# Optimization experiments

Measured on AMD Instinct MI355X. Metric: run time of the kernel, lower is better.

The kernel has to match this reference:

```python
import jax, jax.numpy as jnp
import numpy as np

ATTENTION_DIM = 256
TEMPERATURE = 1.0
NEG_INF = -2.0**32 + 1.0  # matches tf code's padding value


def setup_inputs() -> dict:
    key = jax.random.key(0)
    k1, k2, k3, k4, k5, k6, k7 = jax.random.split(key, 7)
    B, Q, M, QD, MD, AD, VD = 8, 2048, 2048, 512, 512, 256, 256
    inputs = jax.random.normal(k1, (B, Q, QD), dtype=jnp.float32)
    memory = jax.random.normal(k2, (B, M, MD), dtype=jnp.float32)
    memory_lengths = jnp.maximum(jax.random.randint(k3, (B,), 0, M + 1), 1).astype(jnp.int32)
    query_lengths = jnp.maximum(jax.random.randint(k4, (B,), 0, Q + 1), 1).astype(jnp.int32)
    s = 0.02
    Wq = jax.random.normal(k5, (QD, AD), dtype=jnp.float32) * s
    Wk = jax.random.normal(k6, (MD, AD), dtype=jnp.float32) * s
    Wv = jax.random.normal(k7, (MD, VD), dtype=jnp.float32) * s
    return {"inputs": inputs, "memory": memory, "memory_lengths": memory_lengths,
            "query_lengths": query_lengths, "Wq": Wq, "Wk": Wk, "Wv": Wv}


def reference(inputs, memory, memory_lengths, query_lengths, Wq, Wk, Wv):
    # Dense projections (no bias). NOTE: original code (faithfully reproduced)
    # computes values with the KEY layer; Wv is unused.
    queries = jnp.einsum('bqd,da->bqa', inputs, Wq)   # [B,Q,AD]
    keys = jnp.einsum('bmd,da->bma', memory, Wk)      # [B,M,AD]
    values = jnp.einsum('bmd,da->bma', memory, Wk)    # [B,M,AD] (bug in source)

    logits = jnp.einsum('bqa,bma->bqm', queries, keys)
    logits = logits / jnp.sqrt(jnp.float32(ATTENTION_DIM)) / TEMPERATURE

    B, Q, _ = inputs.shape
    M = memory.shape[1]
    mem_mask = jnp.arange(M)[None, :] < memory_lengths[:, None]   # [B,M]
    qry_mask = jnp.arange(Q)[None, :] < query_lengths[:, None]    # [B,Q]
    length_mask = qry_mask[:, :, None] & mem_mask[:, None, :]     # [B,Q,M]

    logits = jnp.where(length_mask, logits, jnp.float32(NEG_INF))
    alignments = jax.nn.softmax(logits, axis=2)                   # [B,Q,M]
    contexts = jnp.einsum('bqm,bma->bqa', alignments, values)     # [B,Q,AD]
    return contexts, alignments
```

## Files before the change

kernel.cpp:

```cpp
#include <hip/hip_runtime.h>
#include <hip/hip_bf16.h>

typedef __attribute__((ext_vector_type(8))) short s8v;
typedef __attribute__((ext_vector_type(4))) float f4v;
typedef __attribute__((ext_vector_type(4))) unsigned short us4;
typedef unsigned short u16;

__device__ __forceinline__ u16 f2bf(float f) {
  union { float f; unsigned int u; } x;
  x.f = f;
  unsigned int lsb = (x.u >> 16) & 1u;
  return (u16)((x.u + 0x7fffu + lsb) >> 16);
}

__device__ __forceinline__ uint4 pack8(float4 a, float4 b) {
  union { u16 u[8]; uint4 v; } t;
  t.u[0] = f2bf(a.x); t.u[1] = f2bf(a.y); t.u[2] = f2bf(a.z); t.u[3] = f2bf(a.w);
  t.u[4] = f2bf(b.x); t.u[5] = f2bf(b.y); t.u[6] = f2bf(b.z); t.u[7] = f2bf(b.w);
  return t.v;
}

__global__ __launch_bounds__(256) void proj_kernel(
    const float* __restrict__ inputs, const float* __restrict__ memory,
    const float* __restrict__ Wq, const float* __restrict__ Wk,
    u16* __restrict__ qb, u16* __restrict__ krow, u16* __restrict__ kcol)
{
  __shared__ u16 Wt[64 * 264];
  __shared__ u16 At[64 * 40];

  const int tid = threadIdx.x;
  const int w = tid >> 6;
  const int l = tid & 63;
  const int lr = l & 15;
  const int lh = l >> 4;
  const int rbase = blockIdx.x * 64;
  const int n0 = blockIdx.y * 64;
  const int src = blockIdx.z;
  const float* __restrict__ A  = src ? memory : inputs;
  const float* __restrict__ Wg = src ? Wk : Wq;

  f4v acc[4];
#pragma unroll
  for (int i = 0; i < 4; ++i) acc[i] = f4v{0.f, 0.f, 0.f, 0.f};

  for (int kh = 0; kh < 2; ++kh) {
    {
      const int kl = tid >> 3;
      const int nl = (tid & 7) * 8;
#pragma unroll
      for (int i = 0; i < 8; ++i) {
        const int k = kl + i * 32;
        const float* s = Wg + (size_t)(kh * 256 + k) * 256 + n0 + nl;
        float4 x0 = *(const float4*)s;
        float4 x1 = *(const float4*)(s + 4);
        Wt[(nl + 0) * 264 + k] = f2bf(x0.x);
        Wt[(nl + 1) * 264 + k] = f2bf(x0.y);
        Wt[(nl + 2) * 264 + k] = f2bf(x0.z);
        Wt[(nl + 3) * 264 + k] = f2bf(x0.w);
        Wt[(nl + 4) * 264 + k] = f2bf(x1.x);
        Wt[(nl + 5) * 264 + k] = f2bf(x1.y);
        Wt[(nl + 6) * 264 + k] = f2bf(x1.z);
        Wt[(nl + 7) * 264 + k] = f2bf(x1.w);
      }
    }
    __syncthreads();
    for (int ks = 0; ks < 8; ++ks) {
      {
        const int row = tid >> 2;
        const int kk = (tid & 3) * 8;
        const float* s = A + (size_t)(rbase + row) * 512 + kh * 256 + ks * 32 + kk;
        float4 x0 = *(const float4*)s;
        float4 x1 = *(const float4*)(s + 4);
        *(uint4*)&At[row * 40 + kk] = pack8(x0, x1);
      }
      __syncthreads();
      const s8v af = *(const s8v*)&At[(w * 16 + lr) * 40 + lh * 8];
#pragma unroll
      for (int nt = 0; nt < 4; ++nt) {
        const s8v bf = *(const s8v*)&Wt[(nt * 16 + lr) * 264 + ks * 32 + lh * 8];
        acc[nt] = __builtin_amdgcn_mfma_f32_16x16x32_bf16(af, bf, acc[nt], 0, 0, 0);
      }
      __syncthreads();
    }
  }

  u16* __restrict__ dst = src ? krow : qb;
#pragma unroll
  for (int nt = 0; nt < 4; ++nt) {
    const int col = n0 + nt * 16 + lr;
    const int R0 = rbase + w * 16 + lh * 4;
    u16 u0 = f2bf(acc[nt][0]);
    u16 u1 = f2bf(acc[nt][1]);
    u16 u2 = f2bf(acc[nt][2]);
    u16 u3 = f2bf(acc[nt][3]);
    dst[(size_t)(R0 + 0) * 256 + col] = u0;
    dst[(size_t)(R0 + 1) * 256 + col] = u1;
    dst[(size_t)(R0 + 2) * 256 + col] = u2;
    dst[(size_t)(R0 + 3) * 256 + col] = u3;
    if (src) {
      const int bb = R0 >> 11;
      const int mm = R0 & 2047;
      us4 pk;
      pk[0] = u0; pk[1] = u1; pk[2] = u2; pk[3] = u3;
      *(us4*)&kcol[((size_t)bb * 256 + col) * 2048 + mm] = pk;
    }
  }
}

__global__ __launch_bounds__(256) void attn_kernel(
    const u16* __restrict__ qb, const u16* __restrict__ krow,
    const u16* __restrict__ kcol, const int* __restrict__ mlens,
    const int* __restrict__ qlens, float* __restrict__ out_ctx,
    float* __restrict__ out_align, float* __restrict__ invsum)
{
  __shared__ u16 kr[32 * 264];
  __shared__ u16 kc[256 * 40];
  __shared__ u16 pl[4 * 16 * 40];

  const int tid = threadIdx.x;
  const int w = tid >> 6;
  const int l = tid & 63;
  const int lr = l & 15;
  const int lh = l >> 4;
  const int b = blockIdx.y;
  const int q0 = blockIdx.x * 64;
  const int mlen = mlens[b];
  const int qlen = qlens[b];
  const int qrow0 = q0 + w * 16 + lh * 4;

  s8v qf[8];
  {
    const u16* qp = qb + ((size_t)b * 2048 + q0 + w * 16 + lr) * 256 + lh * 8;
#pragma unroll
    for (int s = 0; s < 8; ++s) qf[s] = *(const s8v*)(qp + s * 32);
  }

  f4v oacc[16];
#pragma unroll
  for (int i = 0; i < 16; ++i) oacc[i] = f4v{0.f, 0.f, 0.f, 0.f};
  float psum[4] = {0.f, 0.f, 0.f, 0.f};

  const float C2 = 0.09016844005556021f;

  for (int m0 = 0; m0 < 2048; m0 += 32) {
#pragma unroll
    for (int i = 0; i < 4; ++i) {
      const int idx = i * 256 + tid;
      const int m = idx >> 5, G = idx & 31;
      uint4 v = *(const uint4*)(krow + (((size_t)b * 2048 + m0 + m) << 8) + G * 8);
      *(uint4*)&kr[m * 264 + G * 8] = v;
      const int a2 = idx >> 2, gm = idx & 3;
      uint4 v2 = *(const uint4*)(kcol + (((size_t)b * 256 + a2) << 11) + m0 + gm * 8);
      *(uint4*)&kc[a2 * 40 + gm * 8] = v2;
    }
    __syncthreads();

    f4v sacc[2];
    sacc[0] = f4v{0.f, 0.f, 0.f, 0.f};
    sacc[1] = f4v{0.f, 0.f, 0.f, 0.f};
#pragma unroll
    for (int s = 0; s < 8; ++s) {
#pragma unroll
      for (int f = 0; f < 2; ++f) {
        const s8v bf = *(const s8v*)&kr[(f * 16 + lr) * 264 + s * 32 + lh * 8];
        sacc[f] = __builtin_amdgcn_mfma_f32_16x16x32_bf16(qf[s], bf, sacc[f], 0, 0, 0);
      }
    }

#pragma unroll
    for (int f = 0; f < 2; ++f) {
      const int m = m0 + f * 16 + lr;
      const bool vm = m < mlen;
#pragma unroll
      for (int r = 0; r < 4; ++r) {
        const int q = qrow0 + r;
        float p = exp2f(sacc[f][r] * C2);
        if (!vm) p = 0.f;
        if (q >= qlen) p = 1.f;
        psum[r] += p;
        out_align[((size_t)b * 2048 + q) * 2048 + m] = p;
        pl[w * 640 + (lh * 4 + r) * 40 + f * 16 + lr] = f2bf(p);
      }
    }

    const s8v pa = *(const s8v*)&pl[w * 640 + lr * 40 + lh * 8];
#pragma unroll
    for (int at = 0; at < 16; ++at) {
      const s8v vf = *(const s8v*)&kc[(at * 16 + lr) * 40 + lh * 8];
      oacc[at] = __builtin_amdgcn_mfma_f32_16x16x32_bf16(pa, vf, oacc[at], 0, 0, 0);
    }
    __syncthreads();
  }

#pragma unroll
  for (int r = 0; r < 4; ++r) {
    float v = psum[r];
    v += __shfl_xor(v, 1);
    v += __shfl_xor(v, 2);
    v += __shfl_xor(v, 4);
    v += __shfl_xor(v, 8);
    psum[r] = 1.0f / v;
  }

#pragma unroll
  for (int at = 0; at < 16; ++at) {
    const int a = at * 16 + lr;
#pragma unroll
    for (int r = 0; r < 4; ++r) {
      out_ctx[((size_t)b * 2048 + qrow0 + r) * 256 + a] = oacc[at][r] * psum[r];
    }
  }
  if (lr == 0) {
#pragma unroll
    for (int r = 0; r < 4; ++r) invsum[(size_t)b * 2048 + qrow0 + r] = psum[r];
  }
}

__global__ __launch_bounds__(256) void norm_kernel(
    float* __restrict__ align, const float* __restrict__ invsum)
{
  const int row = blockIdx.x;
  const float inv = invsum[row];
  float4* p = (float4*)(align + (size_t)row * 2048);
  const int t = threadIdx.x;
#pragma unroll
  for (int i = 0; i < 2; ++i) {
    float4 v = p[i * 256 + t];
    v.x *= inv; v.y *= inv; v.z *= inv; v.w *= inv;
    p[i * 256 + t] = v;
  }
}

extern "C" void kernel_launch(void* const* d_in, const int* in_sizes, int n_in,
                              void* d_out, int out_size, void* d_ws, size_t ws_size,
                              hipStream_t stream) {
  const float* inputs = (const float*)d_in[0];
  const float* memory = (const float*)d_in[1];
  const int* mlens    = (const int*)d_in[2];
  const int* qlens    = (const int*)d_in[3];
  const float* Wq     = (const float*)d_in[4];
  const float* Wk     = (const float*)d_in[5];
  (void)in_sizes; (void)n_in; (void)out_size; (void)ws_size;

  u16* wsu = (u16*)d_ws;
  u16* qb   = wsu;
  u16* krow = wsu + 4194304;
  u16* kcol = wsu + 8388608;
  float* invsum = (float*)(wsu + 12582912);

  float* out_ctx = (float*)d_out;
  float* out_align = out_ctx + 4194304;

  proj_kernel<<<dim3(256, 4, 2), dim3(256), 0, stream>>>(
      inputs, memory, Wq, Wk, qb, krow, kcol);
  attn_kernel<<<dim3(32, 8), dim3(256), 0, stream>>>(
      qb, krow, kcol, mlens, qlens, out_ctx, out_align, invsum);
  norm_kernel<<<dim3(16384), dim3(256), 0, stream>>>(out_align, invsum);
}
```

Baseline: 201.8 us.

## Split attention into sum pass and split-M write pass, dropping normalize pass

```diff
diff --git a/kernel.cpp b/kernel.cpp
--- a/kernel.cpp
+++ b/kernel.cpp
@@ -107,15 +107,12 @@
   }
 }
 
-__global__ __launch_bounds__(256) void attn_kernel(
+__global__ __launch_bounds__(256) void attn_sum_kernel(
     const u16* __restrict__ qb, const u16* __restrict__ krow,
-    const u16* __restrict__ kcol, const int* __restrict__ mlens,
-    const int* __restrict__ qlens, float* __restrict__ out_ctx,
-    float* __restrict__ out_align, float* __restrict__ invsum)
+    const int* __restrict__ mlens, const int* __restrict__ qlens,
+    float* __restrict__ psum_p)
 {
   __shared__ u16 kr[32 * 264];
-  __shared__ u16 kc[256 * 40];
-  __shared__ u16 pl[4 * 16 * 40];
 
   const int tid = threadIdx.x;
   const int w = tid >> 6;
@@ -124,6 +121,8 @@
   const int lh = l >> 4;
   const int b = blockIdx.y;
   const int q0 = blockIdx.x * 64;
+  const int ms = blockIdx.z;
+  const int m_base = ms * 512;
   const int mlen = mlens[b];
   const int qlen = qlens[b];
   const int qrow0 = q0 + w * 16 + lh * 4;
@@ -135,14 +134,109 @@
     for (int s = 0; s < 8; ++s) qf[s] = *(const s8v*)(qp + s * 32);
   }
 
+  float psum[4] = {0.f, 0.f, 0.f, 0.f};
+  const float C2 = 0.09016844005556021f;
+
+  for (int mo = 0; mo < 512; mo += 32) {
+    const int m0 = m_base + mo;
+#pragma unroll
+    for (int i = 0; i < 4; ++i) {
+      const int idx = i * 256 + tid;
+      const int m = idx >> 5, G = idx & 31;
+      uint4 v = *(const uint4*)(krow + (((size_t)b * 2048 + m0 + m) << 8) + G * 8);
+      *(uint4*)&kr[m * 264 + G * 8] = v;
+    }
+    __syncthreads();
+
+    f4v sacc[2];
+    sacc[0] = f4v{0.f, 0.f, 0.f, 0.f};
+    sacc[1] = f4v{0.f, 0.f, 0.f, 0.f};
+#pragma unroll
+    for (int s = 0; s < 8; ++s) {
+#pragma unroll
+      for (int f = 0; f < 2; ++f) {
+        const s8v bf = *(const s8v*)&kr[(f * 16 + lr) * 264 + s * 32 + lh * 8];
+        sacc[f] = __builtin_amdgcn_mfma_f32_16x16x32_bf16(qf[s], bf, sacc[f], 0, 0, 0);
+      }
+    }
+#pragma unroll
+    for (int f = 0; f < 2; ++f) {
+      const int m = m0 + f * 16 + lr;
+      const bool vm = m < mlen;
+#pragma unroll
+      for (int r = 0; r < 4; ++r) {
+        float p = exp2f(sacc[f][r] * C2);
+        if (!vm) p = 0.f;
+        if (qrow0 + r >= qlen) p = 1.f;
+        psum[r] += p;
+      }
+    }
+    __syncthreads();
+  }
+
+#pragma unroll
+  for (int r = 0; r < 4; ++r) {
+    float v = psum[r];
+    v += __shfl_xor(v, 1);
+    v += __shfl_xor(v, 2);
+    v += __shfl_xor(v, 4);
+    v += __shfl_xor(v, 8);
+    psum[r] = v;
+  }
+  if (lr == 0) {
+#pragma unroll
+    for (int r = 0; r < 4; ++r)
+      psum_p[ms * 16384 + b * 2048 + qrow0 + r] = psum[r];
+  }
+}
+
+__global__ __launch_bounds__(256) void attn_wr_kernel(
+    const u16* __restrict__ qb, const u16* __restrict__ krow,
+    const u16* __restrict__ kcol, const int* __restrict__ mlens,
+    const int* __restrict__ qlens, const float* __restrict__ psum_p,
+    float* __restrict__ out_align, float* __restrict__ octx0,
+    float* __restrict__ octx1)
+{
+  __shared__ u16 kr[32 * 264];
+  __shared__ u16 kc[256 * 40];
+  __shared__ u16 pl[4 * 16 * 40];
+
+  const int tid = threadIdx.x;
+  const int w = tid >> 6;
+  const int l = tid & 63;
+  const int lr = l & 15;
+  const int lh = l >> 4;
+  const int b = blockIdx.y;
+  const int q0 = blockIdx.x * 64;
+  const int mh = blockIdx.z;
+  const int m_base = mh * 1024;
+  const int mlen = mlens[b];
+  const int qlen = qlens[b];
+  const int qrow0 = q0 + w * 16 + lh * 4;
+
+  s8v qf[8];
+  {
+    const u16* qp = qb + ((size_t)b * 2048 + q0 + w * 16 + lr) * 256 + lh * 8;
+#pragma unroll
+    for (int s = 0; s < 8; ++s) qf[s] = *(const s8v*)(qp + s * 32);
+  }
+
+  float inv[4];
+#pragma unroll
+  for (int r = 0; r < 4; ++r) {
+    const int q = b * 2048 + qrow0 + r;
+    float s = psum_p[q] + psum_p[16384 + q] + psum_p[32768 + q] + psum_p[49152 + q];
+    inv[r] = 1.0f / s;
+  }
+
   f4v oacc[16];
 #pragma unroll
   for (int i = 0; i < 16; ++i) oacc[i] = f4v{0.f, 0.f, 0.f, 0.f};
-  float psum[4] = {0.f, 0.f, 0.f, 0.f};
 
   const float C2 = 0.09016844005556021f;
 
-  for (int m0 = 0; m0 < 2048; m0 += 32) {
+  for (int mo = 0; mo < 1024; mo += 32) {
+    const int m0 = m_base + mo;
 #pragma unroll
     for (int i = 0; i < 4; ++i) {
       const int idx = i * 256 + tid;
@@ -177,9 +271,9 @@
         float p = exp2f(sacc[f][r] * C2);
         if (!vm) p = 0.f;
         if (q >= qlen) p = 1.f;
-        psum[r] += p;
-        out_align[((size_t)b * 2048 + q) * 2048 + m] = p;
-        pl[w * 640 + (lh * 4 + r) * 40 + f * 16 + lr] = f2bf(p);
+        const float pn = p * inv[r];
+        __builtin_nontemporal_store(pn, &out_align[((size_t)b * 2048 + q) * 2048 + m]);
+        pl[w * 640 + (lh * 4 + r) * 40 + f * 16 + lr] = f2bf(pn);
       }
     }
 
@@ -192,43 +286,26 @@
     __syncthreads();
   }
 
-#pragma unroll
-  for (int r = 0; r < 4; ++r) {
-    float v = psum[r];
-    v += __shfl_xor(v, 1);
-    v += __shfl_xor(v, 2);
-    v += __shfl_xor(v, 4);
-    v += __shfl_xor(v, 8);
-    psum[r] = 1.0f / v;
-  }
-
+  float* __restrict__ dst = mh ? octx1 : octx0;
 #pragma unroll
   for (int at = 0; at < 16; ++at) {
     const int a = at * 16 + lr;
 #pragma unroll
     for (int r = 0; r < 4; ++r) {
-      out_ctx[((size_t)b * 2048 + qrow0 + r) * 256 + a] = oacc[at][r] * psum[r];
-    }
-  }
-  if (lr == 0) {
-#pragma unroll
-    for (int r = 0; r < 4; ++r) invsum[(size_t)b * 2048 + qrow0 + r] = psum[r];
-  }
-}
-
-__global__ __launch_bounds__(256) void norm_kernel(
-    float* __restrict__ align, const float* __restrict__ invsum)
+      __builtin_nontemporal_store(oacc[at][r],
+          &dst[((size_t)b * 2048 + qrow0 + r) * 256 + a]);
+    }
+  }
+}
+
+__global__ __launch_bounds__(256) void combine_kernel(
+    float* __restrict__ out_ctx, const float* __restrict__ octx1)
 {
-  const int row = blockIdx.x;
-  const float inv = invsum[row];
-  float4* p = (float4*)(align + (size_t)row * 2048);
-  const int t = threadIdx.x;
-#pragma unroll
-  for (int i = 0; i < 2; ++i) {
-    float4 v = p[i * 256 + t];
-    v.x *= inv; v.y *= inv; v.z *= inv; v.w *= inv;
-    p[i * 256 + t] = v;
-  }
+  const size_t i = (size_t)blockIdx.x * 256 + threadIdx.x;
+  float4 a = ((const float4*)out_ctx)[i];
+  float4 c = ((const float4*)octx1)[i];
+  a.x += c.x; a.y += c.y; a.z += c.z; a.w += c.w;
+  ((float4*)out_ctx)[i] = a;
 }
 
 extern "C" void kernel_launch(void* const* d_in, const int* in_sizes, int n_in,
@@ -238,22 +315,25 @@
   const float* memory = (const float*)d_in[1];
   const int* mlens    = (const int*)d_in[2];
   const int* qlens    = (const int*)d_in[3];
+  (void)in_sizes; (void)n_in; (void)out_size; (void)ws_size;
   const float* Wq     = (const float*)d_in[4];
   const float* Wk     = (const float*)d_in[5];
-  (void)in_sizes; (void)n_in; (void)out_size; (void)ws_size;
 
   u16* wsu = (u16*)d_ws;
   u16* qb   = wsu;
   u16* krow = wsu + 4194304;
   u16* kcol = wsu + 8388608;
-  float* invsum = (float*)(wsu + 12582912);
+  float* psum_p = (float*)(wsu + 12582912);
+  float* octx1  = psum_p + 65536;
 
   float* out_ctx = (float*)d_out;
   float* out_align = out_ctx + 4194304;
 
   proj_kernel<<<dim3(256, 4, 2), dim3(256), 0, stream>>>(
       inputs, memory, Wq, Wk, qb, krow, kcol);
-  attn_kernel<<<dim3(32, 8), dim3(256), 0, stream>>>(
-      qb, krow, kcol, mlens, qlens, out_ctx, out_align, invsum);
-  norm_kernel<<<dim3(16384), dim3(256), 0, stream>>>(out_align, invsum);
-}
+  attn_sum_kernel<<<dim3(32, 8, 4), dim3(256), 0, stream>>>(
+      qb, krow, mlens, qlens, psum_p);
+  attn_wr_kernel<<<dim3(32, 8, 2), dim3(256), 0, stream>>>(
+      qb, krow, kcol, mlens, qlens, psum_p, out_align, out_ctx, octx1);
+  combine_kernel<<<dim3(4096), dim3(256), 0, stream>>>(out_ctx, octx1);
+}
```

Measured after the change: 179.3 us. 11.2% less time.

## Split attention into score/sum pass, split-M PV pass, and combine kernel

Applied to the files above, without the earlier changes.

```diff
diff --git a/kernel.cpp b/kernel.cpp
--- a/kernel.cpp
+++ b/kernel.cpp
@@ -11,6 +11,12 @@
   x.f = f;
   unsigned int lsb = (x.u >> 16) & 1u;
   return (u16)((x.u + 0x7fffu + lsb) >> 16);
+}
+
+__device__ __forceinline__ float bf2f(u16 u) {
+  union { unsigned int i; float f; } x;
+  x.i = ((unsigned int)u) << 16;
+  return x.f;
 }
 
 __device__ __forceinline__ uint4 pack8(float4 a, float4 b) {
@@ -107,14 +113,12 @@
   }
 }
 
-__global__ __launch_bounds__(256) void attn_kernel(
+__global__ __launch_bounds__(256) void attn_sum_kernel(
     const u16* __restrict__ qb, const u16* __restrict__ krow,
-    const u16* __restrict__ kcol, const int* __restrict__ mlens,
-    const int* __restrict__ qlens, float* __restrict__ out_ctx,
-    float* __restrict__ out_align, float* __restrict__ invsum)
+    const int* __restrict__ mlens, const int* __restrict__ qlens,
+    float* __restrict__ psum_p, u16* __restrict__ pb)
 {
   __shared__ u16 kr[32 * 264];
-  __shared__ u16 kc[256 * 40];
   __shared__ u16 pl[4 * 16 * 40];
 
   const int tid = threadIdx.x;
@@ -124,6 +128,8 @@
   const int lh = l >> 4;
   const int b = blockIdx.y;
   const int q0 = blockIdx.x * 64;
+  const int ms = blockIdx.z;
+  const int m_base = ms * 512;
   const int mlen = mlens[b];
   const int qlen = qlens[b];
   const int qrow0 = q0 + w * 16 + lh * 4;
@@ -135,23 +141,17 @@
     for (int s = 0; s < 8; ++s) qf[s] = *(const s8v*)(qp + s * 32);
   }
 
-  f4v oacc[16];
-#pragma unroll
-  for (int i = 0; i < 16; ++i) oacc[i] = f4v{0.f, 0.f, 0.f, 0.f};
   float psum[4] = {0.f, 0.f, 0.f, 0.f};
-
   const float C2 = 0.09016844005556021f;
 
-  for (int m0 = 0; m0 < 2048; m0 += 32) {
+  for (int mo = 0; mo < 512; mo += 32) {
+    const int m0 = m_base + mo;
 #pragma unroll
     for (int i = 0; i < 4; ++i) {
       const int idx = i * 256 + tid;
       const int m = idx >> 5, G = idx & 31;
       uint4 v = *(const uint4*)(krow + (((size_t)b * 2048 + m0 + m) << 8) + G * 8);
       *(uint4*)&kr[m * 264 + G * 8] = v;
-      const int a2 = idx >> 2, gm = idx & 3;
-      uint4 v2 = *(const uint4*)(kcol + (((size_t)b * 256 + a2) << 11) + m0 + gm * 8);
-      *(uint4*)&kc[a2 * 40 + gm * 8] = v2;
     }
     __syncthreads();
 
@@ -173,22 +173,16 @@
       const bool vm = m < mlen;
 #pragma unroll
       for (int r = 0; r < 4; ++r) {
-        const int q = qrow0 + r;
         float p = exp2f(sacc[f][r] * C2);
         if (!vm) p = 0.f;
-        if (q >= qlen) p = 1.f;
+        if (qrow0 + r >= qlen) p = 1.f;
         psum[r] += p;
-        out_align[((size_t)b * 2048 + q) * 2048 + m] = p;
         pl[w * 640 + (lh * 4 + r) * 40 + f * 16 + lr] = f2bf(p);
       }
     }
 
-    const s8v pa = *(const s8v*)&pl[w * 640 + lr * 40 + lh * 8];
-#pragma unroll
-    for (int at = 0; at < 16; ++at) {
-      const s8v vf = *(const s8v*)&kc[(at * 16 + lr) * 40 + lh * 8];
-      oacc[at] = __builtin_amdgcn_mfma_f32_16x16x32_bf16(pa, vf, oacc[at], 0, 0, 0);
-    }
+    const s8v pav = *(const s8v*)&pl[w * 640 + lr * 40 + lh * 8];
+    *(s8v*)(pb + ((size_t)b * 2048 + q0 + w * 16 + lr) * 2048 + m0 + lh * 8) = pav;
     __syncthreads();
   }
 
@@ -199,36 +193,106 @@
     v += __shfl_xor(v, 2);
     v += __shfl_xor(v, 4);
     v += __shfl_xor(v, 8);
-    psum[r] = 1.0f / v;
-  }
-
-#pragma unroll
-  for (int at = 0; at < 16; ++at) {
-    const int a = at * 16 + lr;
+    psum[r] = v;
+  }
+  if (lr == 0) {
+#pragma unroll
+    for (int r = 0; r < 4; ++r)
+      psum_p[ms * 16384 + b * 2048 + qrow0 + r] = psum[r];
+  }
+}
+
+__global__ __launch_bounds__(256) void pv_kernel(
+    const u16* __restrict__ pb, const u16* __restrict__ kcol,
+    const float* __restrict__ psum_p, float* __restrict__ out_align,
+    float* __restrict__ out_ctx, float* __restrict__ octx_ws)
+{
+  __shared__ u16 kc[256 * 40];
+
+  const int tid = threadIdx.x;
+  const int w = tid >> 6;
+  const int wq = w >> 1;
+  const int wa = w & 1;
+  const int l = tid & 63;
+  const int lr = l & 15;
+  const int lh = l >> 4;
+  const int b = blockIdx.y;
+  const int qb32 = blockIdx.x * 32;
+  const int mh = blockIdx.z;
+  const int mstart = (mh == 0) ? 0 : (mh == 1 ? 704 : 1376);
+  const int mcount = (mh == 0) ? 704 : 672;
+
+  const int qa = qb32 + wq * 16 + lr;
+  float inv_a;
+  {
+    const int q = b * 2048 + qa;
+    inv_a = 1.0f / (psum_p[q] + psum_p[16384 + q] + psum_p[32768 + q] + psum_p[49152 + q]);
+  }
+  float inv_c[4];
+#pragma unroll
+  for (int r = 0; r < 4; ++r) {
+    const int q = b * 2048 + qb32 + wq * 16 + lh * 4 + r;
+    inv_c[r] = 1.0f / (psum_p[q] + psum_p[16384 + q] + psum_p[32768 + q] + psum_p[49152 + q]);
+  }
+
+  f4v oacc[8];
+#pragma unroll
+  for (int i = 0; i < 8; ++i) oacc[i] = f4v{0.f, 0.f, 0.f, 0.f};
+
+  for (int mo = 0; mo < mcount; mo += 32) {
+    const int m0 = mstart + mo;
+#pragma unroll
+    for (int i = 0; i < 4; ++i) {
+      const int idx = i * 256 + tid;
+      const int a2 = idx >> 2, gm = idx & 3;
+      uint4 v2 = *(const uint4*)(kcol + (((size_t)b * 256 + a2) << 11) + m0 + gm * 8);
+      *(uint4*)&kc[a2 * 40 + gm * 8] = v2;
+    }
+    __syncthreads();
+
+    const s8v pa = *(const s8v*)(pb + ((size_t)b * 2048 + qa) * 2048 + m0 + lh * 8);
+
+    if (wa == 0) {
+      f4v f0, f1;
+      f0[0] = bf2f((u16)pa[0]) * inv_a; f0[1] = bf2f((u16)pa[1]) * inv_a;
+      f0[2] = bf2f((u16)pa[2]) * inv_a; f0[3] = bf2f((u16)pa[3]) * inv_a;
+      f1[0] = bf2f((u16)pa[4]) * inv_a; f1[1] = bf2f((u16)pa[5]) * inv_a;
+      f1[2] = bf2f((u16)pa[6]) * inv_a; f1[3] = bf2f((u16)pa[7]) * inv_a;
+      float* ap = out_align + ((size_t)b * 2048 + qa) * 2048 + m0 + lh * 8;
+      __builtin_nontemporal_store(f0, (f4v*)ap);
+      __builtin_nontemporal_store(f1, (f4v*)(ap + 4));
+    }
+
+#pragma unroll
+    for (int at = 0; at < 8; ++at) {
+      const s8v vf = *(const s8v*)&kc[(wa * 128 + at * 16 + lr) * 40 + lh * 8];
+      oacc[at] = __builtin_amdgcn_mfma_f32_16x16x32_bf16(pa, vf, oacc[at], 0, 0, 0);
+    }
+    __syncthreads();
+  }
+
+  float* __restrict__ dst = (mh == 0) ? out_ctx : (octx_ws + (size_t)(mh - 1) * 4194304);
+#pragma unroll
+  for (int at = 0; at < 8; ++at) {
+    const int a = wa * 128 + at * 16 + lr;
 #pragma unroll
     for (int r = 0; r < 4; ++r) {
-      out_ctx[((size_t)b * 2048 + qrow0 + r) * 256 + a] = oacc[at][r] * psum[r];
-    }
-  }
-  if (lr == 0) {
-#pragma unroll
-    for (int r = 0; r < 4; ++r) invsum[(size_t)b * 2048 + qrow0 + r] = psum[r];
-  }
-}
-
-__global__ __launch_bounds__(256) void norm_kernel(
-    float* __restrict__ align, const float* __restrict__ invsum)
+      __builtin_nontemporal_store(oacc[at][r] * inv_c[r],
+          &dst[((size_t)b * 2048 + qb32 + wq * 16 + lh * 4 + r) * 256 + a]);
+    }
+  }
+}
+
+__global__ __launch_bounds__(256) void combine_kernel(
+    float* __restrict__ out_ctx, const float* __restrict__ octx_ws)
 {
-  const int row = blockIdx.x;
-  const float inv = invsum[row];
-  float4* p = (float4*)(align + (size_t)row * 2048);
-  const int t = threadIdx.x;
-#pragma unroll
-  for (int i = 0; i < 2; ++i) {
-    float4 v = p[i * 256 + t];
-    v.x *= inv; v.y *= inv; v.z *= inv; v.w *= inv;
-    p[i * 256 + t] = v;
-  }
+  const size_t i = (size_t)blockIdx.x * 256 + threadIdx.x;
+  float4 a = ((const float4*)out_ctx)[i];
+  float4 c0 = ((const float4*)octx_ws)[i];
+  float4 c1 = ((const float4*)(octx_ws + 4194304))[i];
+  a.x += c0.x + c1.x; a.y += c0.y + c1.y;
+  a.z += c0.z + c1.z; a.w += c0.w + c1.w;
+  ((float4*)out_ctx)[i] = a;
 }
 
 extern "C" void kernel_launch(void* const* d_in, const int* in_sizes, int n_in,
@@ -246,14 +310,18 @@
   u16* qb   = wsu;
   u16* krow = wsu + 4194304;
   u16* kcol = wsu + 8388608;
-  float* invsum = (float*)(wsu + 12582912);
+  float* psum_p = (float*)(wsu + 12582912);
+  u16* pbuf = wsu + 12713984;
+  float* octx_ws = (float*)(wsu + 46268416);
 
   float* out_ctx = (float*)d_out;
   float* out_align = out_ctx + 4194304;
 
   proj_kernel<<<dim3(256, 4, 2), dim3(256), 0, stream>>>(
       inputs, memory, Wq, Wk, qb, krow, kcol);
-  attn_kernel<<<dim3(32, 8), dim3(256), 0, stream>>>(
-      qb, krow, kcol, mlens, qlens, out_ctx, out_align, invsum);
-  norm_kernel<<<dim3(16384), dim3(256), 0, stream>>>(out_align, invsum);
-}
+  attn_sum_kernel<<<dim3(32, 8, 4), dim3(256), 0, stream>>>(
+      qb, krow, mlens, qlens, psum_p, pbuf);
+  pv_kernel<<<dim3(64, 8, 3), dim3(256), 0, stream>>>(
+      pbuf, kcol, psum_p, out_align, out_ctx, octx_ws);
+  combine_kernel<<<dim3(4096), dim3(256), 0, stream>>>(out_ctx, octx_ws);
+}
```

Result: faster. 189.3 us (-6.2%).
